# Performance work log

Measured on AMD Instinct MI355X. Metric: run time of the kernel, lower is better.

Reference implementation:

```python
import jax, jax.numpy as jnp
import numpy as np

HOP = 512
FAC = 4
FRAME_LEN = FAC * HOP  # 2048
ALPHA = 0.65
BETA = 0.06


def _inverse_stft_window():
    # torch.hann_window (periodic): w[n] = 0.5*(1 - cos(2*pi*n/N))
    n = np.arange(FRAME_LEN)
    w = 0.5 * (1.0 - np.cos(2.0 * np.pi * n / FRAME_LEN))
    denom = w ** 2
    # overlaps = ceil(frame_length / hop) == FAC (frame_length = FAC*HOP exactly)
    denom = denom.reshape(FAC, HOP).sum(axis=0)          # [HOP]
    denom = np.tile(denom, FAC)                          # [FRAME_LEN]
    return (w / denom).astype(np.float32)


def setup_inputs() -> dict:
    key = jax.random.key(0)
    B, F, T = 8, 1024, 2048
    stft_frames = jax.random.normal(key, (B, 2, F, T), dtype=jnp.float32)
    inv_window = jnp.asarray(_inverse_stft_window())
    return {"stft_frames": stft_frames, "inv_window": inv_window}


def reference(stft_frames, inv_window):
    # stft_frames: [B, 2, F, T] (real/imag stacked on dim 1)
    x = jnp.pad(stft_frames, ((0, 0), (0, 0), (0, 1), (0, 0)))  # F -> F+1 (Nyquist bin)
    real = x[:, 0] / BETA   # [B, F+1, T]
    imag = x[:, 1] / BETA
    # denormalize_complex: |x|^(1/alpha) * exp(i * atan2(im, re))
    mag = (real * real + imag * imag) ** (0.5 / ALPHA)
    theta = jnp.arctan2(imag, real)
    spec = jax.lax.complex(mag * jnp.cos(theta), mag * jnp.sin(theta))  # [B, F+1, T]
    frames = jnp.fft.irfft(spec, axis=-2)                 # [B, 2F, T], 2F == FRAME_LEN
    frames = jnp.transpose(frames, (0, 2, 1))             # [B, T, L]
    frames = frames * inv_window[None, None, :]
    B, T, L = frames.shape
    total = (T - 1) * HOP + L
    # vectorized overlap-add (scatter-add replacing the per-frame python loop)
    idx = (jnp.arange(T)[:, None] * HOP + jnp.arange(L)[None, :]).reshape(-1)  # [T*L]
    full = jnp.zeros((B, total), frames.dtype).at[:, idx].add(frames.reshape(B, -1))
    # output_buffer is empty on the first call; chunk = first hop*T samples
    return full[:, : HOP * T]
```

## Files before the change

kernel.cpp:

```cpp
#include <hip/hip_runtime.h>
#include <cstddef>


#define TDIM 2048
#define FDIM 1024
#define TT 8
#define NTOT (512 * 2048)

static constexpr int kBREV[32] = {0,16,8,24,4,20,12,28,2,18,10,26,6,22,14,30,
                                  1,17,9,25,5,21,13,29,3,19,11,27,7,23,15,31};
static constexpr float kTR[16] = {
  1.0f, 0.98078528040323044f, 0.92387953251128674f, 0.83146961230254524f,
  0.70710678118654757f, 0.55557023301960218f, 0.38268343236508978f, 0.19509032201612825f,
  0.0f, -0.19509032201612825f, -0.38268343236508978f, -0.55557023301960218f,
  -0.70710678118654757f, -0.83146961230254524f, -0.92387953251128674f, -0.98078528040323044f};
static constexpr float kTI[16] = {
  0.0f, 0.19509032201612825f, 0.38268343236508978f, 0.55557023301960218f,
  0.70710678118654757f, 0.83146961230254524f, 0.92387953251128674f, 0.98078528040323044f,
  1.0f, 0.98078528040323044f, 0.92387953251128674f, 0.83146961230254524f,
  0.70710678118654757f, 0.55557023301960218f, 0.38268343236508978f, 0.19509032201612825f};

template <int H>
__device__ __forceinline__ void fft32_stage(float ar[32], float ai[32]) {
  constexpr int TSTEP = 16 / H;
  #pragma unroll
  for (int g = 0; g < 32; g += 2 * H) {
    #pragma unroll
    for (int j = 0; j < H; ++j) {
      const float twr = kTR[j * TSTEP];
      const float twi = kTI[j * TSTEP];
      const int i0 = g + j, i1 = i0 + H;
      const float tr = twr * ar[i1] - twi * ai[i1];
      const float ti = twr * ai[i1] + twi * ar[i1];
      ar[i1] = ar[i0] - tr; ai[i1] = ai[i0] - ti;
      ar[i0] += tr;         ai[i0] += ti;
    }
  }
}

__device__ __forceinline__ void ifft32_core(float ar[32], float ai[32]) {
  fft32_stage<1>(ar, ai);
  fft32_stage<2>(ar, ai);
  fft32_stage<4>(ar, ai);
  fft32_stage<8>(ar, ai);
  fft32_stage<16>(ar, ai);
}

__device__ __forceinline__ float pow_gain(float v, float PE, float KS) {
  return KS * __builtin_amdgcn_exp2f(PE * __builtin_amdgcn_logf(v));
}

#define XIDX(t, k1, r) ((k1) * 264 + (r) * 8 + (t))
#define FSTR 2053

__global__ __launch_bounds__(256) void istft_fused(const float* __restrict__ in,
                                                   const float* __restrict__ invw,
                                                   float* __restrict__ out) {
  __shared__ float buf[16896];
  float* Xr = buf;
  float* Xi = buf + 8448;

  const int tid = threadIdx.x;
  const int tl  = tid & 7;
  const int q   = tid >> 3;

  const int id   = blockIdx.x;
  const int xcd  = id & 7;
  const int slot = id >> 3;
  const int b    = slot >> 5;
  const int tile = xcd * 32 + (slot & 31);
  const int t0   = tile * TT;
  const int t    = t0 + tl;

  const float* re_p = in + ((size_t)b * 2 + 0) * ((size_t)FDIM * TDIM);
  const float* im_p = in + ((size_t)b * 2 + 1) * ((size_t)FDIM * TDIM);

  const float KS = (float)(exp((-1.0 / 0.65) * log(0.06)) / 2048.0);
  const float PE = 7.0f / 26.0f;

  {
    float ar[32], ai[32];
    #pragma unroll
    for (int k2 = 0; k2 < 32; ++k2) {
      const int k  = q + 32 * k2;
      const int km = (1024 - k) & 1023;
      const float x1 = re_p[(size_t)k  * TDIM + t];
      const float y1 = im_p[(size_t)k  * TDIM + t];
      const float x2 = re_p[(size_t)km * TDIM + t];
      const float y2 = im_p[(size_t)km * TDIM + t];
      const float g1 = pow_gain(x1 * x1 + y1 * y1, PE, KS);
      const float g2 = pow_gain(x2 * x2 + y2 * y2, PE, KS);
      const float s1r = x1 * g1, s1i = y1 * g1;
      const float s2r = x2 * g2, s2i = y2 * g2;
      const float ang = 3.0679615757712824e-3f * (float)k;
      const float sn = __sinf(ang), cs = __cosf(ang);
      const float Pre = s1r + s2r, Pim = s1i - s2i;
      const float Qre = s1r - s2r, Qim = s1i + s2i;
      const float u = cs * Qim + sn * Qre;
      const float v = cs * Qre - sn * Qim;
      float wr = Pre - u, wi = Pim + v;
      if (q == 0 && k2 == 0) { wr = s1r; wi = s1r; }
      ar[kBREV[k2]] = wr; ai[kBREV[k2]] = wi;
    }
    ifft32_core(ar, ai);
    #pragma unroll
    for (int r = 0; r < 32; ++r) {
      const float ang = 6.1359231515425649e-3f * (float)(q * r);
      const float sn = __sinf(ang), cs = __cosf(ang);
      Xr[XIDX(tl, q, r)] = cs * ar[r] - sn * ai[r];
      Xi[XIDX(tl, q, r)] = cs * ai[r] + sn * ar[r];
    }
  }
  __syncthreads();

  {
    float zr[32], zi[32];
    #pragma unroll
    for (int i = 0; i < 32; ++i) {
      zr[i] = Xr[XIDX(tl, kBREV[i], q)];
      zi[i] = Xi[XIDX(tl, kBREV[i], q)];
    }
    __syncthreads();
    ifft32_core(zr, zi);
    #pragma unroll
    for (int s = 0; s < 32; ++s) {
      const int m  = q + 32 * s;
      const int l0 = 2 * m;
      buf[tl * FSTR + l0]     = zr[s] * invw[l0];
      buf[tl * FSTR + l0 + 1] = zi[s] * invw[l0 + 1];
    }
  }
  __syncthreads();

  float* ob = out + (size_t)b * NTOT;
  for (int rel = 0; rel < 11; ++rel) {
    const int tp = t0 + rel;
    if (tp > 2047) break;
    #pragma unroll
    for (int half = 0; half < 2; ++half) {
      const int j = tid + 256 * half;
      float v = 0.0f;
      #pragma unroll
      for (int c = 0; c < 4; ++c) {
        const int tt = rel - c;
        if (tt >= 0 && tt < TT) v += buf[tt * FSTR + j + 512 * c];
      }
      const int n = tp * 512 + j;
      if (rel >= 3 && rel <= 7) ob[n] = v;
      else atomicAdd(&ob[n], v);
    }
  }
}

extern "C" void kernel_launch(void* const* d_in, const int* in_sizes, int n_in,
                              void* d_out, int out_size, void* d_ws, size_t ws_size,
                              hipStream_t stream) {
  (void)in_sizes; (void)n_in; (void)d_ws; (void)ws_size;
  const float* in   = (const float*)d_in[0];
  const float* invw = (const float*)d_in[1];
  float* out = (float*)d_out;
  hipMemsetAsync(out, 0, (size_t)out_size * sizeof(float), stream);
  istft_fused<<<dim3(TDIM / TT * 8), 256, 0, stream>>>(in, invw, out);
}
```

Measured before the change: 240.7 us.

## Halve shared memory by staging transpose and overlap-add in two passes

Cuts the shared buffer from about 66KB to 33KB by doing the FFT transpose and the overlap-add in two halves. Each half reuses the same LDS region, and partial sums are kept in registers (acc[11][2]). Launch bounds now request 4 blocks per CU to raise occupancy. It also replaces the per-k sin/cos with a constant-table angle-addition rotation. The cost is extra __syncthreads barriers, more live registers (ar/ai, zr/zi and acc all held at once), and idle threads during each half of the transpose load.

```diff
diff --git a/kernel.cpp b/kernel.cpp
--- a/kernel.cpp
+++ b/kernel.cpp
@@ -19,6 +19,24 @@
   0.70710678118654757f, 0.83146961230254524f, 0.92387953251128674f, 0.98078528040323044f,
   1.0f, 0.98078528040323044f, 0.92387953251128674f, 0.83146961230254524f,
   0.70710678118654757f, 0.55557023301960218f, 0.38268343236508978f, 0.19509032201612825f};
+static constexpr float kCC[32] = {
+  1.0f, 0.99518472667219693f, 0.98078528040323044f, 0.95694033573220882f,
+  0.92387953251128674f, 0.88192126434835505f, 0.83146961230254524f, 0.77301045336273699f,
+  0.70710678118654757f, 0.63439328416364549f, 0.55557023301960218f, 0.47139673682599764f,
+  0.38268343236508978f, 0.29028467725446233f, 0.19509032201612825f, 0.098017140329560604f,
+  0.0f, -0.098017140329560604f, -0.19509032201612825f, -0.29028467725446233f,
+  -0.38268343236508978f, -0.47139673682599764f, -0.55557023301960218f, -0.63439328416364549f,
+  -0.70710678118654757f, -0.77301045336273699f, -0.83146961230254524f, -0.88192126434835505f,
+  -0.92387953251128674f, -0.95694033573220882f, -0.98078528040323044f, -0.99518472667219693f};
+static constexpr float kSS[32] = {
+  0.0f, 0.098017140329560604f, 0.19509032201612825f, 0.29028467725446233f,
+  0.38268343236508978f, 0.47139673682599764f, 0.55557023301960218f, 0.63439328416364549f,
+  0.70710678118654757f, 0.77301045336273699f, 0.83146961230254524f, 0.88192126434835505f,
+  0.92387953251128674f, 0.95694033573220882f, 0.98078528040323044f, 0.99518472667219693f,
+  1.0f, 0.99518472667219693f, 0.98078528040323044f, 0.95694033573220882f,
+  0.92387953251128674f, 0.88192126434835505f, 0.83146961230254524f, 0.77301045336273699f,
+  0.70710678118654757f, 0.63439328416364549f, 0.55557023301960218f, 0.47139673682599764f,
+  0.38268343236508978f, 0.29028467725446233f, 0.19509032201612825f, 0.098017140329560604f};
 
 template <int H>
 __device__ __forceinline__ void fft32_stage(float ar[32], float ai[32]) {
@@ -50,15 +68,16 @@
   return KS * __builtin_amdgcn_exp2f(PE * __builtin_amdgcn_logf(v));
 }
 
-#define XIDX(t, k1, r) ((k1) * 264 + (r) * 8 + (t))
-#define FSTR 2053
-
-__global__ __launch_bounds__(256) void istft_fused(const float* __restrict__ in,
-                                                   const float* __restrict__ invw,
-                                                   float* __restrict__ out) {
-  __shared__ float buf[16896];
-  float* Xr = buf;
-  float* Xi = buf + 8448;
+#define XH(t, k1, rh) ((k1) * 132 + (rh) * 8 + (t))
+#define FST2 1029
+
+__global__ __launch_bounds__(256, 4) void istft_fused(const float* __restrict__ in,
+                                                      const float* __restrict__ invw,
+                                                      float* __restrict__ out) {
+  __shared__ float buf[8448];
+  float* Xhr = buf;
+  float* Xhi = buf + 4224;
+  float* Fh  = buf;
 
   const int tid = threadIdx.x;
   const int tl  = tid & 7;
@@ -78,8 +97,10 @@
   const float KS = (float)(exp((-1.0 / 0.65) * log(0.06)) / 2048.0);
   const float PE = 7.0f / 26.0f;
 
+  float ar[32], ai[32];
   {
-    float ar[32], ai[32];
+    const float aq = 3.0679615757712824e-3f * (float)q;
+    const float wc = __cosf(aq), ws = __sinf(aq);
     #pragma unroll
     for (int k2 = 0; k2 < 32; ++k2) {
       const int k  = q + 32 * k2;
@@ -92,8 +113,8 @@
       const float g2 = pow_gain(x2 * x2 + y2 * y2, PE, KS);
       const float s1r = x1 * g1, s1i = y1 * g1;
       const float s2r = x2 * g2, s2i = y2 * g2;
-      const float ang = 3.0679615757712824e-3f * (float)k;
-      const float sn = __sinf(ang), cs = __cosf(ang);
+      const float cs = wc * kCC[k2] - ws * kSS[k2];
+      const float sn = ws * kCC[k2] + wc * kSS[k2];
       const float Pre = s1r + s2r, Pim = s1i - s2i;
       const float Qre = s1r - s2r, Qim = s1i + s2i;
       const float u = cs * Qim + sn * Qre;
@@ -103,47 +124,90 @@
       ar[kBREV[k2]] = wr; ai[kBREV[k2]] = wi;
     }
     ifft32_core(ar, ai);
-    #pragma unroll
-    for (int r = 0; r < 32; ++r) {
-      const float ang = 6.1359231515425649e-3f * (float)(q * r);
-      const float sn = __sinf(ang), cs = __cosf(ang);
-      Xr[XIDX(tl, q, r)] = cs * ar[r] - sn * ai[r];
-      Xi[XIDX(tl, q, r)] = cs * ai[r] + sn * ar[r];
-    }
-  }
-  __syncthreads();
-
-  {
-    float zr[32], zi[32];
+  }
+
+  float zr[32], zi[32];
+  #pragma unroll
+  for (int r = 0; r < 16; ++r) {
+    const float ang = 6.1359231515425649e-3f * (float)(q * r);
+    const float sn = __sinf(ang), cs = __cosf(ang);
+    Xhr[XH(tl, q, r)] = cs * ar[r] - sn * ai[r];
+    Xhi[XH(tl, q, r)] = cs * ai[r] + sn * ar[r];
+  }
+  __syncthreads();
+  if (q < 16) {
     #pragma unroll
     for (int i = 0; i < 32; ++i) {
-      zr[i] = Xr[XIDX(tl, kBREV[i], q)];
-      zi[i] = Xi[XIDX(tl, kBREV[i], q)];
-    }
-    __syncthreads();
-    ifft32_core(zr, zi);
-    #pragma unroll
-    for (int s = 0; s < 32; ++s) {
-      const int m  = q + 32 * s;
-      const int l0 = 2 * m;
-      buf[tl * FSTR + l0]     = zr[s] * invw[l0];
-      buf[tl * FSTR + l0 + 1] = zi[s] * invw[l0 + 1];
-    }
-  }
-  __syncthreads();
+      zr[i] = Xhr[XH(tl, kBREV[i], q)];
+      zi[i] = Xhi[XH(tl, kBREV[i], q)];
+    }
+  }
+  __syncthreads();
+  #pragma unroll
+  for (int r = 16; r < 32; ++r) {
+    const float ang = 6.1359231515425649e-3f * (float)(q * r);
+    const float sn = __sinf(ang), cs = __cosf(ang);
+    Xhr[XH(tl, q, r - 16)] = cs * ar[r] - sn * ai[r];
+    Xhi[XH(tl, q, r - 16)] = cs * ai[r] + sn * ar[r];
+  }
+  __syncthreads();
+  if (q >= 16) {
+    #pragma unroll
+    for (int i = 0; i < 32; ++i) {
+      zr[i] = Xhr[XH(tl, kBREV[i], q - 16)];
+      zi[i] = Xhi[XH(tl, kBREV[i], q - 16)];
+    }
+  }
+  __syncthreads();
+
+  ifft32_core(zr, zi);
 
   float* ob = out + (size_t)b * NTOT;
+  float acc[11][2] = {};
+
+  #pragma unroll
+  for (int s = 0; s < 16; ++s) {
+    const int l0 = 2 * q + 64 * s;
+    Fh[tl * FST2 + l0]     = zr[s] * invw[l0];
+    Fh[tl * FST2 + l0 + 1] = zi[s] * invw[l0 + 1];
+  }
+  __syncthreads();
+  #pragma unroll
   for (int rel = 0; rel < 11; ++rel) {
-    const int tp = t0 + rel;
-    if (tp > 2047) break;
+    if (t0 + rel > 2047) continue;
     #pragma unroll
     for (int half = 0; half < 2; ++half) {
       const int j = tid + 256 * half;
       float v = 0.0f;
       #pragma unroll
-      for (int c = 0; c < 4; ++c) {
+      for (int c = 0; c < 2; ++c) {
         const int tt = rel - c;
-        if (tt >= 0 && tt < TT) v += buf[tt * FSTR + j + 512 * c];
+        if (tt >= 0 && tt < TT) v += Fh[tt * FST2 + j + 512 * c];
+      }
+      acc[rel][half] = v;
+    }
+  }
+  __syncthreads();
+  #pragma unroll
+  for (int s = 16; s < 32; ++s) {
+    const int l0 = 2 * q + 64 * s;
+    const int lp = l0 - 1024;
+    Fh[tl * FST2 + lp]     = zr[s] * invw[l0];
+    Fh[tl * FST2 + lp + 1] = zi[s] * invw[l0 + 1];
+  }
+  __syncthreads();
+  #pragma unroll
+  for (int rel = 0; rel < 11; ++rel) {
+    const int tp = t0 + rel;
+    if (tp > 2047) continue;
+    #pragma unroll
+    for (int half = 0; half < 2; ++half) {
+      const int j = tid + 256 * half;
+      float v = acc[rel][half];
+      #pragma unroll
+      for (int c = 2; c < 4; ++c) {
+        const int tt = rel - c;
+        if (tt >= 0 && tt < TT) v += Fh[tt * FST2 + j + 512 * (c - 2)];
       }
       const int n = tp * 512 + j;
       if (rel >= 3 && rel <= 7) ob[n] = v;
```

After: 271.0 us. +12.6%, slower.
